# Kernel tuning notes

Measured on AMD Instinct MI355X. Metric: run time of the kernel, lower is better.

## Reference

```python
import jax, jax.numpy as jnp
from jax import lax
import numpy as np

EPS_START, EPS_END, EPS_DECAY = 1.0, 0.05, 10000.0


def gru_step(x, h, w_ih, w_hh, b_ih, b_hh):
    # PyTorch GRUCell math; gates stacked as [r, z, n]
    gi = x @ w_ih.T + b_ih
    gh = h @ w_hh.T + b_hh
    i_r, i_z, i_n = jnp.split(gi, 3, axis=1)
    h_r, h_z, h_n = jnp.split(gh, 3, axis=1)
    r = jax.nn.sigmoid(i_r + h_r)
    z = jax.nn.sigmoid(i_z + h_z)
    n = jnp.tanh(i_n + r * h_n)
    return (1.0 - z) * n + z * h


def setup_inputs() -> dict:
    key = jax.random.key(0)
    ks = jax.random.split(key, 7)
    V, E, H = 32000, 256, 512
    s = 0.05
    return {
        "embedding": jax.random.normal(ks[0], (V, E), jnp.float32) * s,
        "w_ih": jax.random.normal(ks[1], (3 * H, E), jnp.float32) * s,
        "w_hh": jax.random.normal(ks[2], (3 * H, H), jnp.float32) * s,
        "b_ih": jax.random.normal(ks[3], (3 * H,), jnp.float32) * s,
        "b_hh": jax.random.normal(ks[4], (3 * H,), jnp.float32) * s,
        "w_out": jax.random.normal(ks[5], (V, H), jnp.float32) * s,
        "b_out": jax.random.normal(ks[6], (V,), jnp.float32) * s,
        "seq_len": 256,
        "batch_size": 512,
    }


def reference(embedding, w_ih, w_hh, b_ih, b_hh, w_out, b_out, seq_len, batch_size):
    V, E = embedding.shape
    H = w_hh.shape[1]
    B = batch_size
    log_unif = jnp.float32(np.log(V))  # -log(vocab_size) fill for epsilon-greedy

    keys = jax.random.split(jax.random.key(42), seq_len)
    ts = jnp.arange(seq_len, dtype=jnp.float32)

    h0 = jnp.zeros((B, H), jnp.float32)
    x0 = jnp.broadcast_to(embedding[0], (B, E))  # start token id 0

    def step(carry, inp):
        h, x = carry
        t, k = inp
        k_eps, k_gum = jax.random.split(k)
        h = gru_step(x, h, w_ih, w_hh, b_ih, b_hh)
        logp = jax.nn.log_softmax(h @ w_out.T + b_out, axis=1)  # [B, V]
        eps_t = EPS_END + (EPS_START - EPS_END) * jnp.exp(-4.0 * t / EPS_DECAY)
        draw = eps_t >= jax.random.uniform(k_eps, (B,))
        masked = jnp.where(draw[:, None], -log_unif, logp)
        g = jax.random.gumbel(k_gum, (B, V), jnp.float32)
        sampled = jnp.argmax(masked + g, axis=1)  # [B] int
        lp = jnp.take_along_axis(logp, sampled[:, None], axis=1)[:, 0]
        x_next = embedding[sampled]
        return (h, x_next), (sampled, lp)

    _, (samples, lps) = lax.scan(step, (h0, x0), (ts, keys))
    return samples.T, lps.T  # [B, S] each
```

## Files before the change

### kernel.cpp

```cpp
#include <hip/hip_runtime.h>
#include <math.h>
#include <stdio.h>

#ifndef JAX_PARTITIONABLE
#define JAX_PARTITIONABLE 1
#endif

namespace {

constexpr int B  = 512;
constexpr int S  = 256;
constexpr int E  = 256;
constexpr int H  = 512;
constexpr int V  = 32000;
constexpr int VBLK = 64;
constexpr int NCH  = V / VBLK;
constexpr int NDMAX = 96;

typedef __bf16 bf16x8 __attribute__((ext_vector_type(8)));
typedef float  f32x4  __attribute__((ext_vector_type(4)));
typedef unsigned u32x4 __attribute__((ext_vector_type(4)));

__device__ __forceinline__ void tf2x32(unsigned k0, unsigned k1,
                                       unsigned x0, unsigned x1,
                                       unsigned& o0, unsigned& o1) {
  unsigned ks2 = k0 ^ k1 ^ 0x1BD11BDAu;
  x0 += k0; x1 += k1;
#define TFR(r) { x0 += x1; x1 = (x1 << (r)) | (x1 >> (32 - (r))); x1 ^= x0; }
  TFR(13) TFR(15) TFR(26) TFR(6)   x0 += k1;  x1 += ks2 + 1u;
  TFR(17) TFR(29) TFR(16) TFR(24)  x0 += ks2; x1 += k0 + 2u;
  TFR(13) TFR(15) TFR(26) TFR(6)   x0 += k0;  x1 += k1 + 3u;
  TFR(17) TFR(29) TFR(16) TFR(24)  x0 += k1;  x1 += ks2 + 4u;
  TFR(13) TFR(15) TFR(26) TFR(6)   x0 += ks2; x1 += k0 + 5u;
#undef TFR
  o0 = x0; o1 = x1;
}

__device__ __forceinline__ unsigned rbits(unsigned g0, unsigned g1,
                                          unsigned b, unsigned v) {
#if JAX_PARTITIONABLE
  unsigned y0, y1;
  tf2x32(g0, g1, 0u, b * (unsigned)V + v, y0, y1);
  return y0 ^ y1;
#else
  const unsigned N2 = (unsigned)(B/2) * (unsigned)V;
  unsigned ii = b * (unsigned)V + v;
  unsigned jj = (b < 256) ? ii : ii - N2;
  unsigned y0, y1;
  tf2x32(g0, g1, jj, N2 + jj, y0, y1);
  return (b < 256) ? y0 : y1;
#endif
}

__device__ __forceinline__ float u01_from_bits(unsigned bits) {
  return __uint_as_float(0x3f800000u | (bits >> 9)) - 1.0f;
}

__device__ __forceinline__ float gumbel_exact(unsigned bits) {
  float u = u01_from_bits(bits);
  if (u == 0.0f) u = 1.1754943508222875e-38f;
  float w = (float)(-log((double)u));
  return (float)(-log((double)w));
}

__device__ __forceinline__ float gumbel_fast(unsigned bits) {
  float u = u01_from_bits(bits);
  if (u == 0.0f) u = 1.1754943508222875e-38f;
  float w = -__logf(u);
  return -__logf(w);
}

__device__ __forceinline__ unsigned short f2bf(float f) {
  unsigned u = __float_as_uint(f);
  unsigned r = (u + 0x7fffu + ((u >> 16) & 1u)) >> 16;
  return (unsigned short)r;
}

__device__ __forceinline__ size_t frag_off(int row, int k, int kTiles) {
  return ((size_t)((row >> 4) * kTiles + (k >> 5)) * 64
          + (row & 15) + 16 * ((k >> 3) & 3)) * 8 + (k & 7);
}

__global__ void k_init_rng(unsigned* __restrict__ kq, unsigned* __restrict__ ke) {
  int t = threadIdx.x;
  unsigned h0, h1, e0, e1, g0, g1;
#if JAX_PARTITIONABLE
  tf2x32(0u, 42u, 0u, (unsigned)t, h0, h1);
  tf2x32(h0, h1, 0u, 0u, e0, e1);
  tf2x32(h0, h1, 0u, 1u, g0, g1);
#else
  unsigned a0, a1, b0, b1;
  if (t < 128) {
    tf2x32(0u, 42u, (unsigned)(2*t),   (unsigned)(256+2*t), a0, a1);
    tf2x32(0u, 42u, (unsigned)(2*t+1), (unsigned)(257+2*t), b0, b1);
    h0 = a0; h1 = b0;
  } else {
    int j = 2*t - 256;
    tf2x32(0u, 42u, (unsigned)j,     (unsigned)(256+j), a0, a1);
    tf2x32(0u, 42u, (unsigned)(j+1), (unsigned)(257+j), b0, b1);
    h0 = a1; h1 = b1;
  }
  unsigned p0, p1, q0, q1;
  tf2x32(h0, h1, 0u, 2u, p0, p1);
  tf2x32(h0, h1, 1u, 3u, q0, q1);
  e0 = p0; e1 = q0; g0 = p1; g1 = q1;
#endif
  ke[2*t] = e0; ke[2*t+1] = e1;
  kq[2*t] = g0; kq[2*t+1] = g1;
}

__global__ void k_init_draws(const unsigned* __restrict__ ke,
                             unsigned char* __restrict__ draws) {
  int t = blockIdx.x;
  int b = threadIdx.x;
  unsigned k0 = ke[2*t], k1 = ke[2*t+1];
  unsigned bits, y0, y1;
#if JAX_PARTITIONABLE
  tf2x32(k0, k1, 0u, (unsigned)b, y0, y1);
  bits = y0 ^ y1;
#else
  if (b < 256) { tf2x32(k0, k1, (unsigned)b,       (unsigned)(256+b), y0, y1); bits = y0; }
  else         { tf2x32(k0, k1, (unsigned)(b-256), (unsigned)b,       y0, y1); bits = y1; }
#endif
  float u   = u01_from_bits(bits);
  float tf  = (float)t;
  float ex  = expf(__fmul_rn(-4.0f, tf) / 10000.0f);
  float eps = __fadd_rn(0.05f, __fmul_rn(0.95f, ex));
  draws[t*B + b] = (eps >= u) ? 1 : 0;
}

__global__ void k_init_nd(const unsigned char* __restrict__ draws,
                          int* __restrict__ nd_slot) {
  int t = blockIdx.x;
  if (threadIdx.x != 0) return;
  int cnt = 0;
  for (int b = 0; b < B; b++) {
    if (!draws[t*B + b] && cnt < NDMAX) nd_slot[t*B + b] = cnt++;
    else nd_slot[t*B + b] = -1;
  }
}

__global__ __launch_bounds__(256) void k_pre_argmax(
    const unsigned* __restrict__ kq, const unsigned char* __restrict__ draws,
    int* __restrict__ pre) {
  const int job  = blockIdx.x * 4 + (threadIdx.x >> 6);
  const int lane = threadIdx.x & 63;
  const int t = job >> 9, b = job & (B - 1);
  if (!draws[t*B + b]) { if (lane == 0) pre[job] = -1; return; }
  const unsigned g0 = kq[2*t], g1 = kq[2*t+1];
  unsigned best = 0u; int bv = V;
  for (int v = lane; v < V; v += 64) {
    unsigned bits = rbits(g0, g1, (unsigned)b, (unsigned)v) >> 9;
    if (bits > best || (bits == best && v < bv)) { best = bits; bv = v; }
  }
#pragma unroll
  for (int m = 1; m < 64; m <<= 1) {
    unsigned ob = __shfl_xor(best, m, 64);
    int      ov = __shfl_xor(bv,   m, 64);
    if (ob > best || (ob == best && ov < bv)) { best = ob; bv = ov; }
  }
  if (lane == 0) pre[job] = bv;
}

__global__ void k_init_state(const float* __restrict__ emb,
                             float* __restrict__ x, float* __restrict__ h) {
  int b = blockIdx.x, tid = threadIdx.x;
  x[b*E + tid] = emb[tid];
  h[b*H + tid] = 0.0f;
  h[b*H + 256 + tid] = 0.0f;
}

__global__ void k_cast_w(const float* __restrict__ w,
                         unsigned short* __restrict__ w_sw) {
  int g = blockIdx.x*256 + threadIdx.x;
  int v  = g >> 6;
  int k0 = (g & 63) * 8;
  const float* src = w + (size_t)v*H + k0;
  union { unsigned short s[8]; u32x4 vv; } u;
#pragma unroll
  for (int e = 0; e < 8; e++) u.s[e] = f2bf(src[e]);
  *(u32x4*)&w_sw[frag_off(v, k0, H/32)] = u.vv;
}

__device__ __forceinline__ float sigm_acc(float v) {
  return (float)(1.0 / (1.0 + exp(-(double)v)));
}
__device__ __forceinline__ float tanh_acc(float v) {
  return (float)tanh((double)v);
}

__global__ __launch_bounds__(256) void k_gates_gru(
    const float* __restrict__ x, const float* __restrict__ hin,
    const float* __restrict__ w_ih, const float* __restrict__ w_hh,
    const float* __restrict__ b_ih, const float* __restrict__ b_hh,
    float* __restrict__ hout, unsigned short* __restrict__ h_sw) {
  __shared__ __align__(16) float As[16][68];
  __shared__ __align__(16) float Ws[16][28];
  const int tid = threadIdx.x;
  const int jj = tid & 7, ty = tid >> 3;
  const int j0 = blockIdx.x * 8;
  const int row0 = blockIdx.y * 64;
  float ai[2][3] = {};
  float ah[2][3] = {};

  for (int k0 = 0; k0 < E; k0 += 16) {
    __syncthreads();
#pragma unroll
    for (int l = 0; l < 4; l++) {
      int idx = tid + l*256;
      int r = idx >> 4, kk = idx & 15;
      As[kk][r] = x[(size_t)(row0 + r)*E + k0 + kk];
    }
#pragma unroll
    for (int l = 0; l < 2; l++) {
      int idx = tid + l*256;
      if (idx < 384) {
        int r = idx >> 4, kk = idx & 15;
        int col = (r >> 3)*512 + j0 + (r & 7);
        Ws[kk][r] = w_ih[(size_t)col*E + k0 + kk];
      }
    }
    __syncthreads();
#pragma unroll
    for (int kk = 0; kk < 16; kk++) {
      float a0 = As[kk][ty], a1 = As[kk][ty + 32];
#pragma unroll
      for (int g = 0; g < 3; g++) {
        float w = Ws[kk][g*8 + jj];
        ai[0][g] = fmaf(a0, w, ai[0][g]);
        ai[1][g] = fmaf(a1, w, ai[1][g]);
      }
    }
  }

  for (int k0 = 0; k0 < H; k0 += 16) {
    __syncthreads();
#pragma unroll
    for (int l = 0; l < 4; l++) {
      int idx = tid + l*256;
      int r = idx >> 4, kk = idx & 15;
      As[kk][r] = hin[(size_t)(row0 + r)*H + k0 + kk];
    }
#pragma unroll
    for (int l = 0; l < 2; l++) {
      int idx = tid + l*256;
      if (idx < 384) {
        int r = idx >> 4, kk = idx & 15;
        int col = (r >> 3)*512 + j0 + (r & 7);
        Ws[kk][r] = w_hh[(size_t)col*H + k0 + kk];
      }
    }
    __syncthreads();
#pragma unroll
    for (int kk = 0; kk < 16; kk++) {
      float a0 = As[kk][ty], a1 = As[kk][ty + 32];
#pragma unroll
      for (int g = 0; g < 3; g++) {
        float w = Ws[kk][g*8 + jj];
        ah[0][g] = fmaf(a0, w, ah[0][g]);
        ah[1][g] = fmaf(a1, w, ah[1][g]);
      }
    }
  }

  const int j = j0 + jj;
#pragma unroll
  for (int i = 0; i < 2; i++) {
    const int b = row0 + ty + i*32;
    float gi_r = __fadd_rn(ai[i][0], b_ih[j]);
    float gi_z = __fadd_rn(ai[i][1], b_ih[512 + j]);
    float gi_n = __fadd_rn(ai[i][2], b_ih[1024 + j]);
    float gh_r = __fadd_rn(ah[i][0], b_hh[j]);
    float gh_z = __fadd_rn(ah[i][1], b_hh[512 + j]);
    float gh_n = __fadd_rn(ah[i][2], b_hh[1024 + j]);
    float r  = sigm_acc(__fadd_rn(gi_r, gh_r));
    float zz = sigm_acc(__fadd_rn(gi_z, gh_z));
    float nn = tanh_acc(__fadd_rn(gi_n, __fmul_rn(r, gh_n)));
    float hv = hin[(size_t)b*H + j];
    float t1 = __fmul_rn(__fsub_rn(1.0f, zz), nn);
    float t2 = __fmul_rn(zz, hv);
    float hn = __fadd_rn(t1, t2);
    hout[(size_t)b*H + j] = hn;
    h_sw[frag_off(b, j, H/32)] = f2bf(hn);
  }
}

__global__ __launch_bounds__(256) void k_mfma_logits(
    const unsigned short* __restrict__ h_sw,
    const unsigned short* __restrict__ w_sw,
    const float* __restrict__ b_out,
    const unsigned* __restrict__ kq,
    const unsigned char* __restrict__ draws,
    int* __restrict__ pre,
    const int* __restrict__ nd_slot_t,
    float* __restrict__ pmax, float* __restrict__ psum,
    float* __restrict__ plog,
    float* __restrict__ nd_keys, float* __restrict__ nd_kmax, int t) {
  const int tid  = threadIdx.x;

  if (blockIdx.y == 0) {
    __shared__ unsigned sb[4];
    __shared__ int      sv[4];
    const int tn = t + 1;
    if (tn >= S) return;
    const int b = blockIdx.x;
    if (!draws[tn*B + b]) { if (tid == 0) pre[tn*B + b] = -1; return; }
    const unsigned g0 = kq[2*tn], g1 = kq[2*tn+1];
    unsigned best = 0u; int bv = V;
    for (int v = tid; v < V; v += 256) {
      unsigned bits = rbits(g0, g1, (unsigned)b, (unsigned)v) >> 9;
      if (bits > best || (bits == best && v < bv)) { best = bits; bv = v; }
    }
#pragma unroll
    for (int m = 1; m < 64; m <<= 1) {
      unsigned ob = __shfl_xor(best, m, 64);
      int      ov = __shfl_xor(bv,   m, 64);
      if (ob > best || (ob == best && ov < bv)) { best = ob; bv = ov; }
    }
    const int wv = tid >> 6;
    if ((tid & 63) == 0) { sb[wv] = best; sv[wv] = bv; }
    __syncthreads();
    if (tid == 0) {
      for (int i = 1; i < 4; i++) {
        unsigned ob = sb[i]; int ov = sv[i];
        if (ob > best || (ob == best && ov < bv)) { best = ob; bv = ov; }
      }
      pre[tn*B + b] = bv;
    }
    return;
  }

  const int L  = (blockIdx.y - 1) * 512 + blockIdx.x;
  const int wg = (L & 7) * 128 + (L >> 3);
  if (wg >= 2*NCH) return;
  const int vblk = wg >> 1;
  const int bblk = wg & 1;
  const int* __restrict__ pre_t = pre + t*B;
  const int lane = tid & 63, w = tid >> 6;
  const int quad = lane >> 4, l15 = lane & 15;

  f32x4 acc[4][4] = {};

  const int mtBase = bblk*16 + w*4;
  const int ntBase = vblk*4;
  const unsigned short* hp = h_sw + (size_t)mtBase*16*512 + lane*8;
  const unsigned short* wp = w_sw + (size_t)ntBase*16*512 + lane*8;

  bf16x8 afc[4], bfc[4];
#pragma unroll
  for (int mt = 0; mt < 4; mt++)
    afc[mt] = __builtin_bit_cast(bf16x8, *(const u32x4*)(hp + (size_t)(mt*16)*512));
#pragma unroll
  for (int nt = 0; nt < 4; nt++)
    bfc[nt] = __builtin_bit_cast(bf16x8, *(const u32x4*)(wp + (size_t)(nt*16)*512));

#pragma unroll 1
  for (int kt = 0; kt < 15; kt++) {
    bf16x8 afn[4], bfn[4];
#pragma unroll
    for (int mt = 0; mt < 4; mt++)
      afn[mt] = __builtin_bit_cast(bf16x8,
          *(const u32x4*)(hp + (size_t)(mt*16 + kt + 1)*512));
#pragma unroll
    for (int nt = 0; nt < 4; nt++)
      bfn[nt] = __builtin_bit_cast(bf16x8,
          *(const u32x4*)(wp + (size_t)(nt*16 + kt + 1)*512));
#pragma unroll
    for (int mt = 0; mt < 4; mt++)
#pragma unroll
      for (int nt = 0; nt < 4; nt++)
        acc[mt][nt] = __builtin_amdgcn_mfma_f32_16x16x32_bf16(
            afc[mt], bfc[nt], acc[mt][nt], 0, 0, 0);
#pragma unroll
    for (int mt = 0; mt < 4; mt++) afc[mt] = afn[mt];
#pragma unroll
    for (int nt = 0; nt < 4; nt++) bfc[nt] = bfn[nt];
  }
  {
#pragma unroll
    for (int mt = 0; mt < 4; mt++)
#pragma unroll
      for (int nt = 0; nt < 4; nt++)
        acc[mt][nt] = __builtin_amdgcn_mfma_f32_16x16x32_bf16(
            afc[mt], bfc[nt], acc[mt][nt], 0, 0, 0);
  }

  const int bW = bblk*256 + w*64;
  const int vW = vblk*64;
  const unsigned g0 = kq[2*t], g1 = kq[2*t+1];
  float bias[4];
#pragma unroll
  for (int nt = 0; nt < 4; nt++) bias[nt] = b_out[vW + nt*16 + l15];

#pragma unroll
  for (int mt = 0; mt < 4; mt++) {
#pragma unroll
    for (int r = 0; r < 4; r++) {
      const int b = bW + mt*16 + quad*4 + r;
      float lg[4];
#pragma unroll
      for (int nt = 0; nt < 4; nt++) lg[nt] = acc[mt][nt][r] + bias[nt];
      float lmax = fmaxf(fmaxf(lg[0], lg[1]), fmaxf(lg[2], lg[3]));
#pragma unroll
      for (int m = 1; m < 16; m <<= 1) lmax = fmaxf(lmax, __shfl_xor(lmax, m, 64));
      float ls = 0.0f;
#pragma unroll
      for (int nt = 0; nt < 4; nt++) ls += __expf(lg[nt] - lmax);
#pragma unroll
      for (int m = 1; m < 16; m <<= 1) ls += __shfl_xor(ls, m, 64);
      if (l15 == 0) { pmax[b*NCH + vblk] = lmax; psum[b*NCH + vblk] = ls; }
      const int pr = pre_t[b];
      if (pr >= 0) {
        int rel = pr - vW;
        if (rel >= 0 && rel < 64 && (rel & 15) == l15) plog[b] = lg[rel >> 4];
      } else {
        const int slot = nd_slot_t[b];
        if (slot >= 0) {
          float key[4];
#pragma unroll
          for (int nt = 0; nt < 4; nt++)
            key[nt] = lg[nt] + gumbel_fast(
                rbits(g0, g1, (unsigned)b, (unsigned)(vW + nt*16 + l15)));
          float* dst = nd_keys + (size_t)slot*V + vW + l15;
#pragma unroll
          for (int nt = 0; nt < 4; nt++) dst[nt*16] = key[nt];
          float kmx = fmaxf(fmaxf(key[0], key[1]), fmaxf(key[2], key[3]));
#pragma unroll
          for (int m = 1; m < 16; m <<= 1) kmx = fmaxf(kmx, __shfl_xor(kmx, m, 64));
          if (l15 == 0) nd_kmax[slot*NCH + vblk] = kmx;
        }
      }
    }
  }
}

__global__ __launch_bounds__(256) void k_finish(
    const float* __restrict__ pmax, const float* __restrict__ psum,
    const float* __restrict__ plog,
    const int* __restrict__ pre_t, const int* __restrict__ nd_slot_t,
    const float* __restrict__ nd_keys, const float* __restrict__ nd_kmax,
    const unsigned* __restrict__ kq,
    const float* __restrict__ h, const float* __restrict__ w_out,
    const float* __restrict__ b_out,
    const float* __restrict__ emb, float* __restrict__ x,
    float* __restrict__ out_samples, float* __restrict__ out_lps, int t) {
  const int b = blockIdx.x;
  const int tid = threadIdx.x;
  __shared__ float sA[256];
  __shared__ int   cand[160];
  __shared__ float cand_key[160], cand_lg[160];
  __shared__ int   ccnt;
  __shared__ int   s_samp;
  __shared__ float s_blog;

  float m = -INFINITY;
  for (int c = tid; c < NCH; c += 256) m = fmaxf(m, pmax[b*NCH + c]);
  sA[tid] = m; __syncthreads();
  for (int s = 128; s > 0; s >>= 1) {
    if (tid < s) sA[tid] = fmaxf(sA[tid], sA[tid+s]);
    __syncthreads();
  }
  const float M = sA[0];
  __syncthreads();
  float sum = 0.0f;
  for (int c = tid; c < NCH; c += 256)
    sum += psum[b*NCH + c] * expf(pmax[b*NCH + c] - M);
  sA[tid] = sum; __syncthreads();
  for (int s = 128; s > 0; s >>= 1) {
    if (tid < s) sA[tid] += sA[tid+s];
    __syncthreads();
  }
  const float SUM = sA[0];
  __syncthreads();

  const int pr = pre_t[b];
  if (pr >= 0) {
    if (tid == 0) { s_samp = pr; s_blog = plog[b]; }
  } else {
    const int slot = nd_slot_t[b];
    if (slot < 0) {
      if (tid == 0) { s_samp = 0; s_blog = plog[b]; }
    } else {
      const unsigned g0 = kq[2*t], g1 = kq[2*t+1];
      if (tid == 0) ccnt = 0;
      float km = -INFINITY;
      for (int c = tid; c < NCH; c += 256) km = fmaxf(km, nd_kmax[slot*NCH + c]);
      sA[tid] = km; __syncthreads();
      for (int s = 128; s > 0; s >>= 1) {
        if (tid < s) sA[tid] = fmaxf(sA[tid], sA[tid+s]);
        __syncthreads();
      }
      const float thr = sA[0] - 0.0859375f;
      __syncthreads();
      const float* keys = nd_keys + (size_t)slot*V;
      for (int c = tid; c < NCH; c += 256) {
        if (nd_kmax[slot*NCH + c] >= thr) {
          for (int j = 0; j < VBLK; j++) {
            float k = keys[c*VBLK + j];
            if (k >= thr) {
              int p = atomicAdd(&ccnt, 1);
              if (p < 160) cand[p] = c*VBLK + j;
            }
          }
        }
      }
      __syncthreads();
      const int nc = min(ccnt, 160);
      const int wid = tid >> 6, lane = tid & 63;
      for (int c = wid; c < nc; c += 4) {
        const int v = cand[c];
        const float* wr = w_out + (size_t)v*H;
        const float* hr = h + (size_t)b*H;
        float s = 0.0f;
#pragma unroll
        for (int i = 0; i < 8; i++) s = fmaf(hr[lane + 64*i], wr[lane + 64*i], s);
#pragma unroll
        for (int mm = 1; mm < 64; mm <<= 1) s += __shfl_xor(s, mm, 64);
        if (lane == 0) {
          float logit = __fadd_rn(s, b_out[v]);
          float key   = __fadd_rn(logit,
                          gumbel_exact(rbits(g0, g1, (unsigned)b, (unsigned)v)));
          cand_key[c] = key; cand_lg[c] = logit;
        }
      }
      __syncthreads();
      if (tid == 0) {
        float bk = -INFINITY; int bv = V; float bl = 0.0f;
        for (int c = 0; c < nc; c++) {
          float k = cand_key[c]; int v = cand[c];
          if (k > bk || (k == bk && v < bv)) { bk = k; bv = v; bl = cand_lg[c]; }
        }
        s_samp = bv; s_blog = bl;
      }
    }
  }
  __syncthreads();
  const int sampled = s_samp;
  if (tid == 0) {
    float lse = (float)log((double)SUM);
    float lp  = __fsub_rn(__fsub_rn(s_blog, M), lse);
    out_samples[b*S + t] = (float)sampled;
    out_lps[b*S + t]     = lp;
  }
  x[b*E + tid] = emb[sampled*E + tid];
}

}

extern "C" void kernel_launch(void* const* d_in, const int* in_sizes, int n_in,
                              void* d_out, int out_size, void* d_ws, size_t ws_size,
                              hipStream_t stream) {
  (void)in_sizes; (void)n_in; (void)out_size;
  const float* emb   = (const float*)d_in[0];
  const float* w_ih  = (const float*)d_in[1];
  const float* w_hh  = (const float*)d_in[2];
  const float* b_ih  = (const float*)d_in[3];
  const float* b_hh  = (const float*)d_in[4];
  const float* w_out = (const float*)d_in[5];
  const float* b_out = (const float*)d_in[6];
  float* out = (float*)d_out;

  char* wsb = (char*)d_ws;
  size_t off = 0;
  auto alloc = [&](size_t nbytes) {
    char* p = wsb + off;
    off += (nbytes + 255) & ~size_t(255);
    return p;
  };
  float* h0    = (float*)alloc((size_t)B*H*4);
  float* h1    = (float*)alloc((size_t)B*H*4);
  float* x     = (float*)alloc((size_t)B*E*4);
  unsigned short* h_sw = (unsigned short*)alloc((size_t)B*H*2);
  unsigned short* w_sw = (unsigned short*)alloc((size_t)V*H*2);
  float* pmax  = (float*)alloc((size_t)B*NCH*4);
  float* psum  = (float*)alloc((size_t)B*NCH*4);
  float* plog  = (float*)alloc((size_t)B*4);
  unsigned* kq = (unsigned*)alloc((size_t)S*2*4);
  unsigned* ke = (unsigned*)alloc((size_t)S*2*4);
  unsigned char* draws = (unsigned char*)alloc((size_t)S*B);
  int* pre     = (int*)alloc((size_t)S*B*4);
  int* nd_slot = (int*)alloc((size_t)S*B*4);
  float* nd_keys = (float*)alloc((size_t)NDMAX*V*4);
  float* nd_kmax = (float*)alloc((size_t)NDMAX*NCH*4);
  if (off > ws_size) {
    fprintf(stderr, "kernel_launch: workspace too small (need %zu, have %zu)\n",
            off, ws_size);
    return;
  }

  k_init_rng<<<1, S, 0, stream>>>(kq, ke);
  k_init_draws<<<S, B, 0, stream>>>(ke, draws);
  k_init_nd<<<S, 64, 0, stream>>>(draws, nd_slot);
  k_pre_argmax<<<B/4, 256, 0, stream>>>(kq, draws, pre);
  k_init_state<<<B, 256, 0, stream>>>(emb, x, h0);
  k_cast_w<<<(V*H/8)/256, 256, 0, stream>>>(w_out, w_sw);

  for (int t = 0; t < S; t++) {
    float* hin  = (t & 1) ? h1 : h0;
    float* hout = (t & 1) ? h0 : h1;
    k_gates_gru<<<dim3(64, 8), 256, 0, stream>>>(x, hin, w_ih, w_hh,
                                                 b_ih, b_hh, hout, h_sw);
    k_mfma_logits<<<dim3(512, 3), 256, 0, stream>>>(
        h_sw, w_sw, b_out, kq, draws, pre, nd_slot + t*B,
        pmax, psum, plog, nd_keys, nd_kmax, t);
    k_finish<<<B, 256, 0, stream>>>(pmax, psum, plog, pre + t*B, nd_slot + t*B,
                                    nd_keys, nd_kmax, kq, hout, w_out, b_out,
                                    emb, x, out, out + (size_t)B*S, t);
  }
}
```

Measured before the change: 39.49 ms.

## Double-buffer GRU gate GEMM tiles and enlarge per-thread register tile

```diff
diff --git a/kernel.cpp b/kernel.cpp
--- a/kernel.cpp
+++ b/kernel.cpp
@@ -194,85 +194,120 @@
     const float* __restrict__ w_ih, const float* __restrict__ w_hh,
     const float* __restrict__ b_ih, const float* __restrict__ b_hh,
     float* __restrict__ hout, unsigned short* __restrict__ h_sw) {
-  __shared__ __align__(16) float As[16][68];
-  __shared__ __align__(16) float Ws[16][28];
+  __shared__ __align__(16) float As[2][16][68];
+  __shared__ __align__(16) float Ws[2][16][52];
   const int tid = threadIdx.x;
-  const int jj = tid & 7, ty = tid >> 3;
-  const int j0 = blockIdx.x * 8;
+  const int jw = tid & 15, rg = tid >> 4;
+  const int j0 = blockIdx.x * 16;
   const int row0 = blockIdx.y * 64;
-  float ai[2][3] = {};
-  float ah[2][3] = {};
-
-  for (int k0 = 0; k0 < E; k0 += 16) {
-    __syncthreads();
-#pragma unroll
-    for (int l = 0; l < 4; l++) {
-      int idx = tid + l*256;
-      int r = idx >> 4, kk = idx & 15;
-      As[kk][r] = x[(size_t)(row0 + r)*E + k0 + kk];
-    }
-#pragma unroll
-    for (int l = 0; l < 2; l++) {
-      int idx = tid + l*256;
-      if (idx < 384) {
-        int r = idx >> 4, kk = idx & 15;
-        int col = (r >> 3)*512 + j0 + (r & 7);
-        Ws[kk][r] = w_ih[(size_t)col*E + k0 + kk];
-      }
-    }
-    __syncthreads();
-#pragma unroll
-    for (int kk = 0; kk < 16; kk++) {
-      float a0 = As[kk][ty], a1 = As[kk][ty + 32];
-#pragma unroll
-      for (int g = 0; g < 3; g++) {
-        float w = Ws[kk][g*8 + jj];
-        ai[0][g] = fmaf(a0, w, ai[0][g]);
-        ai[1][g] = fmaf(a1, w, ai[1][g]);
-      }
-    }
-  }
-
-  for (int k0 = 0; k0 < H; k0 += 16) {
-    __syncthreads();
-#pragma unroll
-    for (int l = 0; l < 4; l++) {
-      int idx = tid + l*256;
-      int r = idx >> 4, kk = idx & 15;
-      As[kk][r] = hin[(size_t)(row0 + r)*H + k0 + kk];
-    }
-#pragma unroll
-    for (int l = 0; l < 2; l++) {
-      int idx = tid + l*256;
-      if (idx < 384) {
-        int r = idx >> 4, kk = idx & 15;
-        int col = (r >> 3)*512 + j0 + (r & 7);
-        Ws[kk][r] = w_hh[(size_t)col*H + k0 + kk];
-      }
-    }
-    __syncthreads();
-#pragma unroll
-    for (int kk = 0; kk < 16; kk++) {
-      float a0 = As[kk][ty], a1 = As[kk][ty + 32];
-#pragma unroll
-      for (int g = 0; g < 3; g++) {
-        float w = Ws[kk][g*8 + jj];
-        ah[0][g] = fmaf(a0, w, ah[0][g]);
-        ah[1][g] = fmaf(a1, w, ah[1][g]);
-      }
-    }
-  }
-
-  const int j = j0 + jj;
-#pragma unroll
-  for (int i = 0; i < 2; i++) {
-    const int b = row0 + ty + i*32;
-    float gi_r = __fadd_rn(ai[i][0], b_ih[j]);
-    float gi_z = __fadd_rn(ai[i][1], b_ih[512 + j]);
-    float gi_n = __fadd_rn(ai[i][2], b_ih[1024 + j]);
-    float gh_r = __fadd_rn(ah[i][0], b_hh[j]);
-    float gh_z = __fadd_rn(ah[i][1], b_hh[512 + j]);
-    float gh_n = __fadd_rn(ah[i][2], b_hh[1024 + j]);
+
+  float ai[4][3] = {};
+  float ah[4][3] = {};
+
+  float pa[4], pw[3];
+#pragma unroll
+  for (int l = 0; l < 4; l++) {
+    int idx = tid + l*256;
+    pa[l] = x[(size_t)(row0 + (idx >> 4))*E + (idx & 15)];
+  }
+#pragma unroll
+  for (int l = 0; l < 3; l++) {
+    int idx = tid + l*256;
+    int c = idx >> 4;
+    pw[l] = w_ih[(size_t)((c >> 4)*512 + j0 + (c & 15))*E + (idx & 15)];
+  }
+#pragma unroll
+  for (int l = 0; l < 4; l++) {
+    int idx = tid + l*256;
+    As[0][idx & 15][idx >> 4] = pa[l];
+  }
+#pragma unroll
+  for (int l = 0; l < 3; l++) {
+    int idx = tid + l*256;
+    Ws[0][idx & 15][idx >> 4] = pw[l];
+  }
+  __syncthreads();
+
+  int p = 0;
+#pragma unroll 1
+  for (int tile = 0; tile < 48; tile++) {
+    if (tile < 47) {
+      const int nt = tile + 1;
+      const float* A = (nt < 16) ? x    : hin;
+      const float* W = (nt < 16) ? w_ih : w_hh;
+      const int   K  = (nt < 16) ? E : H;
+      const int   k0 = (nt < 16) ? nt*16 : (nt - 16)*16;
+#pragma unroll
+      for (int l = 0; l < 4; l++) {
+        int idx = tid + l*256;
+        pa[l] = A[(size_t)(row0 + (idx >> 4))*K + k0 + (idx & 15)];
+      }
+#pragma unroll
+      for (int l = 0; l < 3; l++) {
+        int idx = tid + l*256;
+        int c = idx >> 4;
+        pw[l] = W[(size_t)((c >> 4)*512 + j0 + (c & 15))*K + k0 + (idx & 15)];
+      }
+    }
+    if (tile < 16) {
+#pragma unroll
+      for (int kk = 0; kk < 16; kk++) {
+        const float4 av = *(const float4*)&As[p][kk][rg*4];
+        const float a[4] = {av.x, av.y, av.z, av.w};
+        const float w0 = Ws[p][kk][jw];
+        const float w1 = Ws[p][kk][16 + jw];
+        const float w2 = Ws[p][kk][32 + jw];
+#pragma unroll
+        for (int i = 0; i < 4; i++) {
+          ai[i][0] = fmaf(a[i], w0, ai[i][0]);
+          ai[i][1] = fmaf(a[i], w1, ai[i][1]);
+          ai[i][2] = fmaf(a[i], w2, ai[i][2]);
+        }
+      }
+    } else {
+#pragma unroll
+      for (int kk = 0; kk < 16; kk++) {
+        const float4 av = *(const float4*)&As[p][kk][rg*4];
+        const float a[4] = {av.x, av.y, av.z, av.w};
+        const float w0 = Ws[p][kk][jw];
+        const float w1 = Ws[p][kk][16 + jw];
+        const float w2 = Ws[p][kk][32 + jw];
+#pragma unroll
+        for (int i = 0; i < 4; i++) {
+          ah[i][0] = fmaf(a[i], w0, ah[i][0]);
+          ah[i][1] = fmaf(a[i], w1, ah[i][1]);
+          ah[i][2] = fmaf(a[i], w2, ah[i][2]);
+        }
+      }
+    }
+    if (tile < 47) {
+#pragma unroll
+      for (int l = 0; l < 4; l++) {
+        int idx = tid + l*256;
+        As[p ^ 1][idx & 15][idx >> 4] = pa[l];
+      }
+#pragma unroll
+      for (int l = 0; l < 3; l++) {
+        int idx = tid + l*256;
+        Ws[p ^ 1][idx & 15][idx >> 4] = pw[l];
+      }
+      __syncthreads();
+      p ^= 1;
+    }
+  }
+
+  const int j = j0 + jw;
+  const float bi_r = b_ih[j], bi_z = b_ih[512 + j], bi_n = b_ih[1024 + j];
+  const float bh_r = b_hh[j], bh_z = b_hh[512 + j], bh_n = b_hh[1024 + j];
+#pragma unroll
+  for (int i = 0; i < 4; i++) {
+    const int b = row0 + rg*4 + i;
+    float gi_r = __fadd_rn(ai[i][0], bi_r);
+    float gi_z = __fadd_rn(ai[i][1], bi_z);
+    float gi_n = __fadd_rn(ai[i][2], bi_n);
+    float gh_r = __fadd_rn(ah[i][0], bh_r);
+    float gh_z = __fadd_rn(ah[i][1], bh_z);
+    float gh_n = __fadd_rn(ah[i][2], bh_n);
     float r  = sigm_acc(__fadd_rn(gi_r, gh_r));
     float zz = sigm_acc(__fadd_rn(gi_z, gh_z));
     float nn = tanh_acc(__fadd_rn(gi_n, __fmul_rn(r, gh_n)));
@@ -598,7 +633,7 @@
   for (int t = 0; t < S; t++) {
     float* hin  = (t & 1) ? h1 : h0;
     float* hout = (t & 1) ? h0 : h1;
-    k_gates_gru<<<dim3(64, 8), 256, 0, stream>>>(x, hin, w_ih, w_hh,
+    k_gates_gru<<<dim3(32, 8), 256, 0, stream>>>(x, hin, w_ih, w_hh,
                                                  b_ih, b_hh, hout, h_sw);
     k_mfma_logits<<<dim3(512, 3), 256, 0, stream>>>(
         h_sw, w_sw, b_out, kq, draws, pre, nd_slot + t*B,
```

Result: faster. 36.73 ms (-7.0%).
